# Kernel tuning notes

Measured on AMD Instinct MI355X. Metric: run time of the kernel, lower is better.

Reference implementation:

```python
import jax, jax.numpy as jnp
import numpy as np

B, L, D, H, K = 32, 2048, 512, 256, 4  # batch, bag_size, input_dim, hidden_dim, n_attentions


def setup_inputs() -> dict:
    key = jax.random.key(0)
    k_x, k1, k1b, k2, k2b, k3, k3b = jax.random.split(key, 7)
    s1 = 1.0 / np.sqrt(D)
    s2 = 1.0 / np.sqrt(H)
    return {
        "x": jax.random.normal(k_x, (B * L, D), dtype=jnp.float32),
        "W1": jax.random.uniform(k1, (D, H), jnp.float32, -s1, s1),
        "b1": jax.random.uniform(k1b, (H,), jnp.float32, -s1, s1),
        "W3": jax.random.uniform(k3, (D, H), jnp.float32, -s1, s1),
        "b3": jax.random.uniform(k3b, (H,), jnp.float32, -s1, s1),
        "W2": jax.random.uniform(k2, (H, K), jnp.float32, -s2, s2),
        "b2": jax.random.uniform(k2b, (K,), jnp.float32, -s2, s2),
        "bag_lengths": jnp.full((B,), L, dtype=jnp.int32),
    }


def reference(x, W1, b1, W3, b3, W2, b2, bag_lengths):
    batch = bag_lengths.shape[0]
    bag = x.shape[0] // batch  # equal-length bags (fast path in original)
    # gated attention MLP, per instance: [N, K]
    A = jnp.tanh(x @ W1 + b1) * jax.nn.sigmoid(x @ W3 + b3)
    A = A @ W2 + b2
    # per-bag softmax over instances, per attention head
    A = A.reshape(batch, bag, K).transpose(0, 2, 1)  # [B, K, L]
    A = jax.nn.softmax(A, axis=2)
    # attention-weighted sum of instances -> [B, K, D] -> [B, K*D]
    out = jnp.einsum('bkl,bld->bkd', A, x.reshape(batch, bag, -1))
    return out.reshape(batch, -1)
```

## Files before the change

### kernel.cpp

```cpp
#include <hip/hip_runtime.h>
#include <hip/hip_bf16.h>


typedef short  bf16x8 __attribute__((ext_vector_type(8)));
typedef float  f32x4  __attribute__((ext_vector_type(4)));

#define D_IN    512
#define H_DIM   256
#define L_BAG   2048
#define XSLAB   520

__device__ __forceinline__ short f2bf(float f) {
  union { __hip_bfloat16 h; short s; } u;
  u.h = __float2bfloat16(f);
  return u.s;
}
__device__ __forceinline__ float bf2f(short s) {
  union { float f; unsigned u; } u;
  u.u = ((unsigned)(unsigned short)s) << 16;
  return u.f;
}

__global__ __launch_bounds__(256) void k_prep_w(const float* __restrict__ W1,
                                                const float* __restrict__ W3,
                                                short* __restrict__ wc) {
  int t = blockIdx.x * 256 + threadIdx.x;
  int n_c = t & 511;
  int kc  = t >> 9;
  int kt = kc >> 2, c = kc & 3;
  int g = n_c >> 5, j = n_c & 31;
  const float* src = (j < 16) ? W1 : W3;
  int h = g * 16 + (j & 15);
  bf16x8 v;
  #pragma unroll
  for (int r = 0; r < 8; ++r) v[r] = f2bf(src[(kc * 8 + r) * H_DIM + h]);
  *(bf16x8*)(wc + kt * 16384 + (c * 512 + n_c) * 8) = v;
}

__global__ __launch_bounds__(512, 4) void k_fused(
    const float* __restrict__ x,
    const short* __restrict__ wc,
    const float* __restrict__ b1, const float* __restrict__ b3,
    const float* __restrict__ W2,
    short* __restrict__ part, float* __restrict__ psumP)
{
  __shared__ __align__(16) short xbf[64 * XSLAB];
  __shared__ float lpart[8][64][4];
  __shared__ __align__(16) float wlds[64 * 4];
  __shared__ float psc[4][4];

  const int tid  = threadIdx.x;
  const int lane = tid & 63;
  const int w    = tid >> 6;
  const int l15  = lane & 15;
  const int q    = lane >> 4;
  const int blk  = blockIdx.x;
  const long row0 = (long)blk * 64;

  {
    const int r   = tid & 63;
    const int kc0 = (tid >> 6) * 8;
    const float* xr = x + (row0 + r) * D_IN + kc0 * 8;
    #pragma unroll
    for (int j = 0; j < 8; ++j) {
      float4 f0 = ((const float4*)(xr + j * 8))[0];
      float4 f1 = ((const float4*)(xr + j * 8))[1];
      bf16x8 v;
      v[0] = f2bf(f0.x); v[1] = f2bf(f0.y); v[2] = f2bf(f0.z); v[3] = f2bf(f0.w);
      v[4] = f2bf(f1.x); v[5] = f2bf(f1.y); v[6] = f2bf(f1.z); v[7] = f2bf(f1.w);
      *(bf16x8*)&xbf[(kc0 + j) * XSLAB + r * 8] = v;
    }
  }
  __syncthreads();

  f32x4 acc[4][4];
  #pragma unroll
  for (int mf = 0; mf < 4; ++mf)
    #pragma unroll
    for (int nf = 0; nf < 4; ++nf) acc[mf][nf] = (f32x4){0.f, 0.f, 0.f, 0.f};

  const short* bgp = wc + (q * 512 + w * 64 + l15) * 8;

  #pragma unroll 1
  for (int kt = 0; kt < 16; ++kt) {
    bf16x8 af[4], bfr[4];
    const short* bk = bgp + kt * 16384;
    #pragma unroll
    for (int nf = 0; nf < 4; ++nf)
      bfr[nf] = *(const bf16x8*)(bk + nf * 128);
    const int ab = (kt * 4 + q) * XSLAB + l15 * 8;
    #pragma unroll
    for (int mf = 0; mf < 4; ++mf)
      af[mf] = *(const bf16x8*)&xbf[ab + mf * 128];
    #pragma unroll
    for (int mf = 0; mf < 4; ++mf)
      #pragma unroll
      for (int nf = 0; nf < 4; ++nf)
        acc[mf][nf] = __builtin_amdgcn_mfma_f32_16x16x32_bf16(af[mf], bfr[nf], acc[mf][nf], 0, 0, 0);
  }

  float b1v[2], b3v[2];
  f32x4 wv[2];
  #pragma unroll
  for (int p = 0; p < 2; ++p) {
    int h = w * 32 + p * 16 + l15;
    b1v[p] = b1[h];
    b3v[p] = b3[h];
    wv[p] = *(const f32x4*)&W2[h * 4];
  }
  #pragma unroll
  for (int mf = 0; mf < 4; ++mf) {
    float pl[4][4];
    #pragma unroll
    for (int j = 0; j < 4; ++j)
      #pragma unroll
      for (int kk = 0; kk < 4; ++kk) pl[j][kk] = 0.f;
    #pragma unroll
    for (int p = 0; p < 2; ++p)
      #pragma unroll
      for (int j = 0; j < 4; ++j) {
        float h1 = acc[mf][2 * p][j]     + b1v[p];
        float h3 = acc[mf][2 * p + 1][j] + b3v[p];
        float th = 1.f - __fdividef(2.f, __expf(2.f * h1) + 1.f);
        float sg = __fdividef(1.f, 1.f + __expf(-h3));
        float g = th * sg;
        pl[j][0] += g * wv[p][0];
        pl[j][1] += g * wv[p][1];
        pl[j][2] += g * wv[p][2];
        pl[j][3] += g * wv[p][3];
      }
    #pragma unroll
    for (int off = 1; off < 16; off <<= 1)
      #pragma unroll
      for (int j = 0; j < 4; ++j)
        #pragma unroll
        for (int kk = 0; kk < 4; ++kk)
          pl[j][kk] += __shfl_xor(pl[j][kk], off);
    if (l15 == 0) {
      #pragma unroll
      for (int j = 0; j < 4; ++j)
        #pragma unroll
        for (int kk = 0; kk < 4; ++kk)
          lpart[w][mf * 16 + q * 4 + j][kk] = pl[j][kk];
    }
  }
  __syncthreads();

  if (tid < 256) {
    const int r = tid >> 2, kk = tid & 3;
    float lg = 0.f;
    #pragma unroll
    for (int ww = 0; ww < 8; ++ww) lg += lpart[ww][r][kk];
    float e = __expf(lg);
    wlds[r * 4 + kk] = e;
    float v = e;
    #pragma unroll
    for (int o = 4; o < 64; o <<= 1) v += __shfl_xor(v, o);
    if (lane < 4) psc[tid >> 6][lane] = v;
  }
  __syncthreads();
  if (tid < 4) psumP[blk * 4 + tid] = psc[0][tid] + psc[1][tid] + psc[2][tid] + psc[3][tid];

  {
    const int d = tid;
    const int xoff = (d >> 3) * XSLAB + (d & 7);
    float a0 = 0.f, a1 = 0.f, a2 = 0.f, a3 = 0.f;
    #pragma unroll 8
    for (int l = 0; l < 64; ++l) {
      float4 wv4 = *(const float4*)&wlds[l * 4];
      float xf = bf2f(xbf[xoff + l * 8]);
      a0 += wv4.x * xf; a1 += wv4.y * xf; a2 += wv4.z * xf; a3 += wv4.w * xf;
    }
    short* pp = part + (long)blk * 2048 + d;
    pp[0]    = f2bf(a0);
    pp[512]  = f2bf(a1);
    pp[1024] = f2bf(a2);
    pp[1536] = f2bf(a3);
  }
}

__global__ __launch_bounds__(256) void k_finalize(const short* __restrict__ part,
                                                  const float* __restrict__ psumP,
                                                  float* __restrict__ out) {
  int idx = blockIdx.x * 256 + threadIdx.x;
  int b = idx >> 11, k = (idx >> 9) & 3, d = idx & 511;
  const short* pb = part + ((long)b * 32) * 2048 + k * 512 + d;
  float s = 0.f, ps = 0.f;
  #pragma unroll
  for (int c = 0; c < 32; ++c) {
    s  += bf2f(pb[c * 2048]);
    ps += psumP[(b * 32 + c) * 4 + k];
  }
  out[idx] = s / ps;
}

extern "C" void kernel_launch(void* const* d_in, const int* in_sizes, int n_in,
                              void* d_out, int out_size, void* d_ws, size_t ws_size,
                              hipStream_t stream) {
  const float* x  = (const float*)d_in[0];
  const float* W1 = (const float*)d_in[1];
  const float* b1 = (const float*)d_in[2];
  const float* W3 = (const float*)d_in[3];
  const float* b3 = (const float*)d_in[4];
  const float* W2 = (const float*)d_in[5];
  float* out = (float*)d_out;

  char* ws = (char*)d_ws;
  short* wc    = (short*)(ws + 0);
  short* part  = (short*)(ws + 524288);
  float* psumP = (float*)(ws + 524288 + 4194304);

  hipLaunchKernelGGL(k_prep_w,   dim3(128),  dim3(256), 0, stream, W1, W3, wc);
  hipLaunchKernelGGL(k_fused,    dim3(1024), dim3(512), 0, stream, x, wc, b1, b3, W2, part, psumP);
  hipLaunchKernelGGL(k_finalize, dim3(256),  dim3(256), 0, stream, part, psumP, out);
}
```

Before: 81.37 us.

## Double-buffer weight fragment loads, drop LDS padding, pool from fp32 global x

```diff
diff --git a/kernel.cpp b/kernel.cpp
--- a/kernel.cpp
+++ b/kernel.cpp
@@ -8,7 +8,6 @@
 #define D_IN    512
 #define H_DIM   256
 #define L_BAG   2048
-#define XSLAB   520
 
 __device__ __forceinline__ short f2bf(float f) {
   union { __hip_bfloat16 h; short s; } u;
@@ -44,7 +43,7 @@
     const float* __restrict__ W2,
     short* __restrict__ part, float* __restrict__ psumP)
 {
-  __shared__ __align__(16) short xbf[64 * XSLAB];
+  __shared__ __align__(16) short xbf[64 * 512];
   __shared__ float lpart[8][64][4];
   __shared__ __align__(16) float wlds[64 * 4];
   __shared__ float psc[4][4];
@@ -68,7 +67,7 @@
       bf16x8 v;
       v[0] = f2bf(f0.x); v[1] = f2bf(f0.y); v[2] = f2bf(f0.z); v[3] = f2bf(f0.w);
       v[4] = f2bf(f1.x); v[5] = f2bf(f1.y); v[6] = f2bf(f1.z); v[7] = f2bf(f1.w);
-      *(bf16x8*)&xbf[(kc0 + j) * XSLAB + r * 8] = v;
+      *(bf16x8*)&xbf[((kc0 + j) * 64 + r) * 8] = v;
     }
   }
   __syncthreads();
@@ -81,22 +80,41 @@
 
   const short* bgp = wc + (q * 512 + w * 64 + l15) * 8;
 
-  #pragma unroll 1
-  for (int kt = 0; kt < 16; ++kt) {
-    bf16x8 af[4], bfr[4];
-    const short* bk = bgp + kt * 16384;
-    #pragma unroll
-    for (int nf = 0; nf < 4; ++nf)
-      bfr[nf] = *(const bf16x8*)(bk + nf * 128);
-    const int ab = (kt * 4 + q) * XSLAB + l15 * 8;
-    #pragma unroll
-    for (int mf = 0; mf < 4; ++mf)
-      af[mf] = *(const bf16x8*)&xbf[ab + mf * 128];
-    #pragma unroll
-    for (int mf = 0; mf < 4; ++mf)
-      #pragma unroll
-      for (int nf = 0; nf < 4; ++nf)
-        acc[mf][nf] = __builtin_amdgcn_mfma_f32_16x16x32_bf16(af[mf], bfr[nf], acc[mf][nf], 0, 0, 0);
+  bf16x8 bA[4], bB[4];
+#define LDBA(kt) { const short* bk_ = bgp + (kt) * 16384; \
+    _Pragma("unroll") for (int f_ = 0; f_ < 4; ++f_) bA[f_] = *(const bf16x8*)(bk_ + f_ * 128); }
+#define LDBB(kt) { const short* bk_ = bgp + (kt) * 16384; \
+    _Pragma("unroll") for (int f_ = 0; f_ < 4; ++f_) bB[f_] = *(const bf16x8*)(bk_ + f_ * 128); }
+
+  LDBA(0);
+  #pragma unroll
+  for (int kp = 0; kp < 8; ++kp) {
+    {
+      const int kt = 2 * kp;
+      const int ab = (kt * 4 + q) * 512 + l15 * 8;
+      bf16x8 af[4];
+      #pragma unroll
+      for (int mf = 0; mf < 4; ++mf) af[mf] = *(const bf16x8*)&xbf[ab + mf * 128];
+      LDBB(kt + 1);
+      #pragma unroll
+      for (int mf = 0; mf < 4; ++mf)
+        #pragma unroll
+        for (int nf = 0; nf < 4; ++nf)
+          acc[mf][nf] = __builtin_amdgcn_mfma_f32_16x16x32_bf16(af[mf], bA[nf], acc[mf][nf], 0, 0, 0);
+    }
+    {
+      const int kt = 2 * kp + 1;
+      const int ab = (kt * 4 + q) * 512 + l15 * 8;
+      bf16x8 af[4];
+      #pragma unroll
+      for (int mf = 0; mf < 4; ++mf) af[mf] = *(const bf16x8*)&xbf[ab + mf * 128];
+      if (kp < 7) LDBA(kt + 1);
+      #pragma unroll
+      for (int mf = 0; mf < 4; ++mf)
+        #pragma unroll
+        for (int nf = 0; nf < 4; ++nf)
+          acc[mf][nf] = __builtin_amdgcn_mfma_f32_16x16x32_bf16(af[mf], bB[nf], acc[mf][nf], 0, 0, 0);
+    }
   }
 
   float b1v[2], b3v[2];
@@ -163,12 +181,12 @@
 
   {
     const int d = tid;
-    const int xoff = (d >> 3) * XSLAB + (d & 7);
+    const float* xg = x + row0 * D_IN + d;
     float a0 = 0.f, a1 = 0.f, a2 = 0.f, a3 = 0.f;
     #pragma unroll 8
     for (int l = 0; l < 64; ++l) {
+      float xf = xg[(long)l * D_IN];
       float4 wv4 = *(const float4*)&wlds[l * 4];
-      float xf = bf2f(xbf[xoff + l * 8]);
       a0 += wv4.x * xf; a1 += wv4.y * xf; a2 += wv4.z * xf; a3 += wv4.w * xf;
     }
     short* pp = part + (long)blk * 2048 + d;
```

Result: slower. 99.13 us (+21.8%).

## Software-pipeline B-fragment loads and remove LDS padding with rotated pooling reads

Applied to the files above, without the earlier changes.

```diff
diff --git a/kernel.cpp b/kernel.cpp
--- a/kernel.cpp
+++ b/kernel.cpp
@@ -8,7 +8,6 @@
 #define D_IN    512
 #define H_DIM   256
 #define L_BAG   2048
-#define XSLAB   520
 
 __device__ __forceinline__ short f2bf(float f) {
   union { __hip_bfloat16 h; short s; } u;
@@ -44,7 +43,7 @@
     const float* __restrict__ W2,
     short* __restrict__ part, float* __restrict__ psumP)
 {
-  __shared__ __align__(16) short xbf[64 * XSLAB];
+  __shared__ __align__(16) short xbf[64 * 512];
   __shared__ float lpart[8][64][4];
   __shared__ __align__(16) float wlds[64 * 4];
   __shared__ float psc[4][4];
@@ -68,7 +67,7 @@
       bf16x8 v;
       v[0] = f2bf(f0.x); v[1] = f2bf(f0.y); v[2] = f2bf(f0.z); v[3] = f2bf(f0.w);
       v[4] = f2bf(f1.x); v[5] = f2bf(f1.y); v[6] = f2bf(f1.z); v[7] = f2bf(f1.w);
-      *(bf16x8*)&xbf[(kc0 + j) * XSLAB + r * 8] = v;
+      *(bf16x8*)&xbf[((kc0 + j) * 64 + r) * 8] = v;
     }
   }
   __syncthreads();
@@ -81,22 +80,31 @@
 
   const short* bgp = wc + (q * 512 + w * 64 + l15) * 8;
 
-  #pragma unroll 1
+  bf16x8 bp0[2], bp1[2];
+#define LDP0(kt) { const short* p_ = bgp + (kt) * 16384; \
+    bp0[0] = *(const bf16x8*)(p_);       bp0[1] = *(const bf16x8*)(p_ + 128); }
+#define LDP1(kt) { const short* p_ = bgp + (kt) * 16384; \
+    bp1[0] = *(const bf16x8*)(p_ + 256); bp1[1] = *(const bf16x8*)(p_ + 384); }
+
+  LDP0(0);
+  #pragma unroll
   for (int kt = 0; kt < 16; ++kt) {
-    bf16x8 af[4], bfr[4];
-    const short* bk = bgp + kt * 16384;
-    #pragma unroll
-    for (int nf = 0; nf < 4; ++nf)
-      bfr[nf] = *(const bf16x8*)(bk + nf * 128);
-    const int ab = (kt * 4 + q) * XSLAB + l15 * 8;
-    #pragma unroll
-    for (int mf = 0; mf < 4; ++mf)
-      af[mf] = *(const bf16x8*)&xbf[ab + mf * 128];
-    #pragma unroll
-    for (int mf = 0; mf < 4; ++mf)
-      #pragma unroll
-      for (int nf = 0; nf < 4; ++nf)
-        acc[mf][nf] = __builtin_amdgcn_mfma_f32_16x16x32_bf16(af[mf], bfr[nf], acc[mf][nf], 0, 0, 0);
+    LDP1(kt);
+    const int ab = (kt * 4 + q) * 512 + l15 * 8;
+    bf16x8 af[4];
+    #pragma unroll
+    for (int mf = 0; mf < 4; ++mf) af[mf] = *(const bf16x8*)&xbf[ab + mf * 128];
+    #pragma unroll
+    for (int mf = 0; mf < 4; ++mf) {
+      acc[mf][0] = __builtin_amdgcn_mfma_f32_16x16x32_bf16(af[mf], bp0[0], acc[mf][0], 0, 0, 0);
+      acc[mf][1] = __builtin_amdgcn_mfma_f32_16x16x32_bf16(af[mf], bp0[1], acc[mf][1], 0, 0, 0);
+    }
+    if (kt < 15) LDP0(kt + 1);
+    #pragma unroll
+    for (int mf = 0; mf < 4; ++mf) {
+      acc[mf][2] = __builtin_amdgcn_mfma_f32_16x16x32_bf16(af[mf], bp1[0], acc[mf][2], 0, 0, 0);
+      acc[mf][3] = __builtin_amdgcn_mfma_f32_16x16x32_bf16(af[mf], bp1[1], acc[mf][3], 0, 0, 0);
+    }
   }
 
   float b1v[2], b3v[2];
@@ -162,13 +170,16 @@
   if (tid < 4) psumP[blk * 4 + tid] = psc[0][tid] + psc[1][tid] + psc[2][tid] + psc[3][tid];
 
   {
-    const int d = tid;
-    const int xoff = (d >> 3) * XSLAB + (d & 7);
+    const int d  = tid;
+    const int kc = d >> 3;
+    const int e  = d & 7;
+    const short* xcol = &xbf[kc * 512 + e];
     float a0 = 0.f, a1 = 0.f, a2 = 0.f, a3 = 0.f;
     #pragma unroll 8
-    for (int l = 0; l < 64; ++l) {
+    for (int i = 0; i < 64; ++i) {
+      int l = (i + kc) & 63;
+      float xf = bf2f(xcol[l * 8]);
       float4 wv4 = *(const float4*)&wlds[l * 4];
-      float xf = bf2f(xbf[xoff + l * 8]);
       a0 += wv4.x * xf; a1 += wv4.y * xf; a2 += wv4.z * xf; a3 += wv4.w * xf;
     }
     short* pp = part + (long)blk * 2048 + d;
```

Result: slower. 86.57 us (+6.4%).
